# Kernel tuning notes

Hardware: AMD Instinct MI355X
Metric: run time of the kernel (lower is better)

The kernel has to match this reference:

```python
import jax, jax.numpy as jnp
import numpy as np

D_MODEL = 1024
NUM_HEADS = 16
D_K = D_MODEL // NUM_HEADS
NEG = -10000.0


def setup_inputs() -> dict:
    key = jax.random.key(0)
    ks = jax.random.split(key, 8)
    B, S = 2, 2048
    query = jax.random.normal(ks[0], (B, S, D_MODEL), dtype=jnp.float32)
    key_t = jax.random.normal(ks[1], (B, S, D_MODEL), dtype=jnp.float32)
    value = jax.random.normal(ks[2], (B, S, D_MODEL), dtype=jnp.float32)
    mask = jax.random.randint(ks[3], (B, S), 0, 2, dtype=jnp.int32)
    scale = 1.0 / np.sqrt(D_MODEL)
    Wq = jax.random.normal(ks[4], (D_MODEL, D_MODEL), dtype=jnp.float32) * scale
    Wk = jax.random.normal(ks[5], (D_MODEL, D_MODEL), dtype=jnp.float32) * scale
    Wv = jax.random.normal(ks[6], (D_MODEL, D_MODEL), dtype=jnp.float32) * scale
    Wo = jax.random.normal(ks[7], (D_MODEL, D_MODEL), dtype=jnp.float32) * scale
    return {"query": query, "key": key_t, "value": value, "mask": mask,
            "Wq": Wq, "Wk": Wk, "Wv": Wv, "Wo": Wo}


def reference(query, key, value, mask, Wq, Wk, Wv, Wo):
    B, Sq, _ = query.shape
    Sk = key.shape[1]
    # Linear projections (torch Linear: x @ W.T), split heads -> [B,H,S,d_k]
    def proj(x, W, S):
        return (x @ W.T).reshape(B, S, NUM_HEADS, D_K).transpose(0, 2, 1, 3)
    Q = proj(query, Wq, Sq)
    K = proj(key, Wk, Sk)
    V = proj(value, Wv, Sk)
    # scores [B,H,Sq,Sk]
    scores = jnp.einsum("bhqd,bhkd->bhqk", Q, K) / jnp.sqrt(jnp.float32(D_K))
    # padding mask [B,Sk] -> [B,1,1,Sk]
    pad = mask[:, None, None, :]
    scores = jnp.where(pad == 0, NEG, scores)
    # causal mask (mask_future=True)
    causal = jnp.tril(jnp.ones((Sq, Sk), dtype=bool))
    scores = jnp.where(causal, scores, NEG)
    probs = jax.nn.softmax(scores, axis=-1)  # dropout p=0.0 -> identity
    out = jnp.einsum("bhqk,bhkd->bhqd", probs, V)
    out = out.transpose(0, 2, 1, 3).reshape(B, Sq, D_MODEL)
    return out @ Wo.T
```

## Files before the change

kernel.cpp:

```cpp
#include <hip/hip_runtime.h>
#include <hip/hip_bf16.h>

typedef __attribute__((ext_vector_type(8))) short s16x8;
typedef __attribute__((ext_vector_type(4))) float f32x4;

#define MFMA16(a,b,c) __builtin_amdgcn_mfma_f32_16x16x32_bf16((a),(b),(c),0,0,0)

#define GLD16(gp, lp) __builtin_amdgcn_global_load_lds( \
  (const __attribute__((address_space(1))) unsigned int*)(gp), \
  (__attribute__((address_space(3))) unsigned int*)(lp), 16, 0, 0)

static __device__ __forceinline__ unsigned short f2bu(float f) {
  __hip_bfloat16 h = __float2bfloat16(f);
  unsigned short u; __builtin_memcpy(&u, &h, 2); return u;
}
static __device__ __forceinline__ float b2f(unsigned short u) {
  unsigned int x = ((unsigned int)u) << 16; float f; __builtin_memcpy(&f, &x, 4); return f;
}

__global__ __launch_bounds__(256) void cast_w4(const float* __restrict__ w0, const float* __restrict__ w1,
                                               const float* __restrict__ w2, const float* __restrict__ w3,
                                               unsigned short* __restrict__ o0, unsigned short* __restrict__ o1,
                                               unsigned short* __restrict__ o2, unsigned short* __restrict__ o3) {
  const int y = blockIdx.y;
  const float* in = (y == 0) ? w0 : (y == 1) ? w1 : (y == 2) ? w2 : w3;
  unsigned short* out = (y == 0) ? o0 : (y == 1) ? o1 : (y == 2) ? o2 : o3;
  int i = blockIdx.x * 256 + threadIdx.x;
  float4 v = *(const float4*)(in + (size_t)i * 4);
  unsigned int p0 = (unsigned int)f2bu(v.x) | ((unsigned int)f2bu(v.y) << 16);
  unsigned int p1 = (unsigned int)f2bu(v.z) | ((unsigned int)f2bu(v.w) << 16);
  uint2 pk; pk.x = p0; pk.y = p1;
  *(uint2*)(out + (size_t)i * 4) = pk;
}

static __device__ __forceinline__ void gemm_core(const float* __restrict__ A,
                                                 const unsigned short* __restrict__ Bw,
                                                 int m0, int n0,
                                                 f32x4 (&acc)[4][4],
                                                 unsigned short (*As)[64], unsigned short (*Bs)[64]) {
  const int K = 1024;
  const int tid = threadIdx.x;
  const int lane = tid & 63, wave = tid >> 6;
  const int wm = wave >> 1, wn = wave & 1;
  const int row16 = lane & 15, kgrp = lane >> 4;
  const int srow = lane >> 3, sslot = (lane & 7) ^ srow;
  const int sw = row16 & 7;

  for (int k0 = 0; k0 < K; k0 += 64) {
#pragma unroll
    for (int i = 0; i < 4; i++) {
      int rr = (wave * 4 + i) * 8 + srow;
      GLD16(Bw + (size_t)(n0 + rr) * K + k0 + sslot * 8,
            (char*)Bs + (wave * 4 + i) * 1024);
    }
    const float* Ag = A + (size_t)m0 * K + k0;
#pragma unroll
    for (int i = 0; i < 8; i++) {
      int f = tid + i * 256;
      int r = f >> 4, c = f & 15;
      float4 v = *(const float4*)(Ag + (size_t)r * K + c * 4);
      unsigned int p0 = (unsigned int)f2bu(v.x) | ((unsigned int)f2bu(v.y) << 16);
      unsigned int p1 = (unsigned int)f2bu(v.z) | ((unsigned int)f2bu(v.w) << 16);
      uint2 pk; pk.x = p0; pk.y = p1;
      int slot = (c >> 1) ^ (r & 7), half = c & 1;
      *(uint2*)((char*)&As[r][0] + slot * 16 + half * 8) = pk;
    }
    __syncthreads();

#pragma unroll
    for (int kk = 0; kk < 2; kk++) {
      s16x8 af[4], bfr[4];
#pragma unroll
      for (int mi = 0; mi < 4; mi++) {
        int rr = wm * 64 + mi * 16 + row16;
        af[mi] = *(const s16x8*)((char*)&As[rr][0] + ((kk * 4 + kgrp) ^ sw) * 16);
      }
#pragma unroll
      for (int ni = 0; ni < 4; ni++) {
        int rr = wn * 64 + ni * 16 + row16;
        bfr[ni] = *(const s16x8*)((char*)&Bs[rr][0] + ((kk * 4 + kgrp) ^ sw) * 16);
      }
#pragma unroll
      for (int mi = 0; mi < 4; mi++)
#pragma unroll
        for (int ni = 0; ni < 4; ni++)
          acc[mi][ni] = MFMA16(af[mi], bfr[ni], acc[mi][ni]);
    }
    __syncthreads();
  }
}

__global__ __launch_bounds__(256) void qkv_gemm(const float* __restrict__ q, const float* __restrict__ k,
                                                const float* __restrict__ v,
                                                const unsigned short* __restrict__ Wqb,
                                                const unsigned short* __restrict__ Wkb,
                                                const unsigned short* __restrict__ Wvb,
                                                unsigned short* __restrict__ Qb,
                                                unsigned short* __restrict__ Kb,
                                                unsigned short* __restrict__ Vt) {
  __shared__ unsigned short As[128][64];
  __shared__ unsigned short Bs[128][64];
  const int xcd = blockIdx.x & 7, u = blockIdx.x >> 3;
  const int g = xcd * 12 + (u >> 3);
  const int z = g >> 5, mstrip = g & 31;
  const int m0 = mstrip * 128, n0 = (u & 7) * 128;

  const float* A = (z == 0) ? q : (z == 1) ? k : v;
  const unsigned short* Bw = (z == 0) ? Wqb : (z == 1) ? Wkb : Wvb;

  f32x4 acc[4][4] = {};
  gemm_core(A, Bw, m0, n0, acc, As, Bs);

  const int lane = threadIdx.x & 63, wave = threadIdx.x >> 6;
  const int wm = wave >> 1, wn = wave & 1;
  const int row16 = lane & 15, kgrp = lane >> 4;

  if (z < 2) {
    unsigned short* C = z ? Kb : Qb;
#pragma unroll
    for (int mi = 0; mi < 4; mi++)
#pragma unroll
      for (int ni = 0; ni < 4; ni++)
#pragma unroll
        for (int r = 0; r < 4; r++) {
          int row = m0 + wm * 64 + mi * 16 + kgrp * 4 + r;
          int col = n0 + wn * 64 + ni * 16 + row16;
          C[(size_t)row * 1024 + col] = f2bu(acc[mi][ni][r]);
        }
  } else {
#pragma unroll
    for (int mi = 0; mi < 4; mi++)
#pragma unroll
      for (int ni = 0; ni < 4; ni++) {
        int mb = m0 + wm * 64 + mi * 16 + kgrp * 4;
        int col = n0 + wn * 64 + ni * 16 + row16;
        int bb = mb >> 11, s = mb & 2047;
        unsigned int p0 = (unsigned int)f2bu(acc[mi][ni][0]) | ((unsigned int)f2bu(acc[mi][ni][1]) << 16);
        unsigned int p1 = (unsigned int)f2bu(acc[mi][ni][2]) | ((unsigned int)f2bu(acc[mi][ni][3]) << 16);
        uint2 pk; pk.x = p0; pk.y = p1;
        *(uint2*)&Vt[(((size_t)(bb * 1024 + col)) << 11) + s] = pk;
      }
  }
}

__global__ __launch_bounds__(256) void gemm_wo(const float* __restrict__ A,
                                               const unsigned short* __restrict__ Bw,
                                               float* __restrict__ C) {
  __shared__ unsigned short As[128][64];
  __shared__ unsigned short Bs[128][64];
  const int xcd = blockIdx.x & 7, u = blockIdx.x >> 3;
  const int g = xcd * 4 + (u >> 3);
  const int m0 = g * 128, n0 = (u & 7) * 128;

  f32x4 acc[4][4] = {};
  gemm_core(A, Bw, m0, n0, acc, As, Bs);

  const int lane = threadIdx.x & 63, wave = threadIdx.x >> 6;
  const int wm = wave >> 1, wn = wave & 1;
  const int row16 = lane & 15, kgrp = lane >> 4;
#pragma unroll
  for (int mi = 0; mi < 4; mi++)
#pragma unroll
    for (int ni = 0; ni < 4; ni++)
#pragma unroll
      for (int r = 0; r < 4; r++) {
        int row = m0 + wm * 64 + mi * 16 + kgrp * 4 + r;
        int col = n0 + wn * 64 + ni * 16 + row16;
        C[(size_t)row * 1024 + col] = acc[mi][ni][r];
      }
}

__global__ __launch_bounds__(256) void fu_kernel(const int* __restrict__ mask, int* __restrict__ fu) {
  const int S = 2048;
  int b = blockIdx.x;
  __shared__ int red[256];
  int best = S;
  for (int k = threadIdx.x; k < S; k += 256)
    if (mask[b * S + k] != 0 && k < best) best = k;
  red[threadIdx.x] = best;
  __syncthreads();
  for (int s = 128; s > 0; s >>= 1) {
    if (threadIdx.x < s) red[threadIdx.x] = min(red[threadIdx.x], red[threadIdx.x + s]);
    __syncthreads();
  }
  if (threadIdx.x == 0) fu[b] = red[0];
}

__global__ __launch_bounds__(256) void reduce_vt(const unsigned short* __restrict__ Vt,
                                                 float* __restrict__ vsum) {
  __shared__ float red[256];
  const unsigned short* p = Vt + ((size_t)blockIdx.x << 11) + threadIdx.x * 8;
  uint4 u = *(const uint4*)p;
  float s = b2f((unsigned short)(u.x & 0xffff));
  s += b2f((unsigned short)(u.x >> 16));
  s += b2f((unsigned short)(u.y & 0xffff));
  s += b2f((unsigned short)(u.y >> 16));
  s += b2f((unsigned short)(u.z & 0xffff));
  s += b2f((unsigned short)(u.z >> 16));
  s += b2f((unsigned short)(u.w & 0xffff));
  s += b2f((unsigned short)(u.w >> 16));
  red[threadIdx.x] = s;
  __syncthreads();
  for (int st = 128; st > 0; st >>= 1) {
    if (threadIdx.x < st) red[threadIdx.x] += red[threadIdx.x + st];
    __syncthreads();
  }
  if (threadIdx.x == 0) vsum[blockIdx.x] = red[0];
}

__global__ __launch_bounds__(256) void flash_attn4(const unsigned short* __restrict__ Q,
                                                   const unsigned short* __restrict__ Kp,
                                                   const unsigned short* __restrict__ Vt,
                                                   const int* __restrict__ mask,
                                                   const int* __restrict__ fu,
                                                   const float* __restrict__ vsum,
                                                   float* __restrict__ O) {
  const int S = 2048, DM = 1024;
  const int xcd = blockIdx.x & 7, idx = blockIdx.x >> 3;
  const int bh = xcd * 4 + (idx >> 4);
  const int pairq = idx & 15;
  const int b = bh >> 4, h = bh & 15;
  const int tid = threadIdx.x, lane = tid & 63, wave = tid >> 6;
  const int row16 = lane & 15, kgrp = lane >> 4;

  __shared__ unsigned short Ks[2][64][64];
  __shared__ unsigned short Vs[2][64][64];
  __shared__ unsigned short Ps[4][16][72];

  const size_t base = ((size_t)b * S) * DM + h * 64;
  const size_t vtb = ((size_t)(b * 1024 + h * 64)) * S;
  const int* maskb = mask + b * S;

  const int srow = lane >> 3;
  const int sslot = (lane & 7) ^ srow;

  const int fub = fu[b];
  const float* vs = vsum + b * DM + h * 64;
  const int sw = row16 & 7;

#pragma unroll
  for (int pass = 0; pass < 2; ++pass) {
    const int qt = pass ? (31 - pairq) : pairq;
    const int q0 = qt * 64 + wave * 16;
    const int qg = q0 + row16;
    const int nt = qt + 1;

    s16x8 qf0 = *(const s16x8*)&Q[base + (size_t)qg * DM + kgrp * 8];
    s16x8 qf1 = *(const s16x8*)&Q[base + (size_t)qg * DM + 32 + kgrp * 8];

    f32x4 oacc[4] = {};
    float m_run = -1e30f, l_run = 0.f;

    auto stage = [&](int t, int bf) {
      const int kb = t * 64;
#pragma unroll
      for (int c2 = 0; c2 < 2; c2++) {
        const int r = wave * 16 + c2 * 8 + srow;
        GLD16(Kp + base + (size_t)(kb + r) * DM + sslot * 8,
              (char*)&Ks[bf][0][0] + (wave * 2 + c2) * 1024);
        GLD16(Vt + vtb + (size_t)r * S + kb + sslot * 8,
              (char*)&Vs[bf][0][0] + (wave * 2 + c2) * 1024);
      }
    };

    stage(0, 0);
    asm volatile("s_waitcnt vmcnt(0)" ::: "memory");
    __syncthreads();

    int cur = 0;
    for (int t = 0; t < nt; ++t) {
      if (t + 1 < nt) stage(t + 1, cur ^ 1);
      const int kb = t * 64;

      f32x4 sc[4];
#pragma unroll
      for (int nf = 0; nf < 4; nf++) {
        const int rr = nf * 16 + row16;
        s16x8 k0 = *(const s16x8*)&Ks[cur][rr][(kgrp ^ sw) * 8];
        s16x8 k1 = *(const s16x8*)&Ks[cur][rr][((4 + kgrp) ^ sw) * 8];
        f32x4 a = {};
        a = MFMA16(k0, qf0, a);
        a = MFMA16(k1, qf1, a);
        sc[nf] = a;
      }

#pragma unroll
      for (int nf = 0; nf < 4; nf++) {
        const int kbase = kb + nf * 16 + kgrp * 4;
        int4 mv = *(const int4*)&maskb[kbase];
#pragma unroll
        for (int r = 0; r < 4; r++) {
          int m_ok = (r == 0) ? mv.x : (r == 1) ? mv.y : (r == 2) ? mv.z : mv.w;
          float s = sc[nf][r] * 0.125f;
          sc[nf][r] = (kbase + r > qg || m_ok == 0) ? -10000.0f : s;
        }
      }

      float t01 = fmaxf(fmaxf(sc[0][0], sc[0][1]), fmaxf(sc[0][2], sc[0][3]));
      float t23 = fmaxf(fmaxf(sc[1][0], sc[1][1]), fmaxf(sc[1][2], sc[1][3]));
      float t45 = fmaxf(fmaxf(sc[2][0], sc[2][1]), fmaxf(sc[2][2], sc[2][3]));
      float t67 = fmaxf(fmaxf(sc[3][0], sc[3][1]), fmaxf(sc[3][2], sc[3][3]));
      float tmax = fmaxf(fmaxf(t01, t23), fmaxf(t45, t67));
      tmax = fmaxf(tmax, __shfl_xor(tmax, 16));
      tmax = fmaxf(tmax, __shfl_xor(tmax, 32));

      float mnew = fmaxf(m_run, tmax);
      float alpha = __expf(m_run - mnew);
      m_run = mnew;

      float rsum = 0.f;
#pragma unroll
      for (int nf = 0; nf < 4; nf++)
#pragma unroll
        for (int r = 0; r < 4; r++) {
          float p = __expf(sc[nf][r] - mnew);
          sc[nf][r] = p;
          rsum += p;
        }
      rsum += __shfl_xor(rsum, 16);
      rsum += __shfl_xor(rsum, 32);
      l_run = l_run * alpha + rsum;
#pragma unroll
      for (int nf2 = 0; nf2 < 4; nf2++)
#pragma unroll
        for (int r = 0; r < 4; r++) oacc[nf2][r] *= alpha;

#pragma unroll
      for (int nf = 0; nf < 4; nf++) {
        uint2 pk;
        pk.x = (unsigned int)f2bu(sc[nf][0]) | ((unsigned int)f2bu(sc[nf][1]) << 16);
        pk.y = (unsigned int)f2bu(sc[nf][2]) | ((unsigned int)f2bu(sc[nf][3]) << 16);
        *(uint2*)&Ps[wave][row16][nf * 16 + kgrp * 4] = pk;
      }
      s16x8 pf0 = *(const s16x8*)&Ps[wave][row16][kgrp * 8];
      s16x8 pf1 = *(const s16x8*)&Ps[wave][row16][32 + kgrp * 8];

#pragma unroll
      for (int nf2 = 0; nf2 < 4; nf2++) {
        const int rr = nf2 * 16 + row16;
        s16x8 v0 = *(const s16x8*)&Vs[cur][rr][(kgrp ^ sw) * 8];
        s16x8 v1 = *(const s16x8*)&Vs[cur][rr][((4 + kgrp) ^ sw) * 8];
        oacc[nf2] = MFMA16(v0, pf0, oacc[nf2]);
        oacc[nf2] = MFMA16(v1, pf1, oacc[nf2]);
      }

      asm volatile("s_waitcnt vmcnt(0)" ::: "memory");
      __syncthreads();
      cur ^= 1;
    }

    const float rl = 1.0f / l_run;
#pragma unroll
    for (int nf2 = 0; nf2 < 4; nf2++) {
      const int d0 = nf2 * 16 + kgrp * 4;
      float4 val;
      val.x = oacc[nf2][0] * rl;
      val.y = oacc[nf2][1] * rl;
      val.z = oacc[nf2][2] * rl;
      val.w = oacc[nf2][3] * rl;
      if (qg < fub) {
        float4 vv = *(const float4*)&vs[d0];
        val.x = vv.x * (1.0f / 2048.0f);
        val.y = vv.y * (1.0f / 2048.0f);
        val.z = vv.z * (1.0f / 2048.0f);
        val.w = vv.w * (1.0f / 2048.0f);
      }
      *(float4*)&O[base + (size_t)qg * DM + d0] = val;
    }
  }
}

extern "C" void kernel_launch(void* const* d_in, const int* in_sizes, int n_in,
                              void* d_out, int out_size, void* d_ws, size_t ws_size,
                              hipStream_t stream) {
  const float* q    = (const float*)d_in[0];
  const float* k    = (const float*)d_in[1];
  const float* v    = (const float*)d_in[2];
  const int*   mask = (const int*)d_in[3];
  const float* Wq   = (const float*)d_in[4];
  const float* Wk   = (const float*)d_in[5];
  const float* Wv   = (const float*)d_in[6];
  const float* Wo   = (const float*)d_in[7];
  float* out = (float*)d_out;
  char* ws = (char*)d_ws;

  unsigned short* Wqb = (unsigned short*)(ws + (size_t)0);
  unsigned short* Wkb = (unsigned short*)(ws + ((size_t)2 << 20));
  unsigned short* Wvb = (unsigned short*)(ws + ((size_t)4 << 20));
  unsigned short* Wob = (unsigned short*)(ws + ((size_t)6 << 20));
  unsigned short* Qb  = (unsigned short*)(ws + ((size_t)8 << 20));
  unsigned short* Kb  = (unsigned short*)(ws + ((size_t)16 << 20));
  unsigned short* Vt  = (unsigned short*)(ws + ((size_t)24 << 20));
  float* attn = (float*)(ws + ((size_t)32 << 20));
  float* vsum = (float*)(ws + ((size_t)48 << 20));
  int*   fub  = (int*)(ws + ((size_t)48 << 20) + (64 << 10));

  cast_w4<<<dim3(1024, 4), 256, 0, stream>>>(Wq, Wk, Wv, Wo, Wqb, Wkb, Wvb, Wob);

  qkv_gemm<<<768, 256, 0, stream>>>(q, k, v, Wqb, Wkb, Wvb, Qb, Kb, Vt);

  fu_kernel<<<2, 256, 0, stream>>>(mask, fub);
  reduce_vt<<<2048, 256, 0, stream>>>(Vt, vsum);

  flash_attn4<<<512, 256, 0, stream>>>(Qb, Kb, Vt, mask, fub, vsum, attn);

  gemm_wo<<<256, 256, 0, stream>>>(attn, Wob, out);
}
```

Before: 159.4 us.

## Pre-cast activations to bf16 and use async LDS loads for both GEMM operands

Adds a single cast kernel that converts q, k, v and all weights to bf16 up front, so gemm_core loads both A and B through global_load_lds instead of loading fp32 A, converting per tile and storing to LDS. The attention output is now written as bf16, which halves its write and the Wo GEMM read. The trade is an extra full read and write pass over the inputs, with buffers aliased into d_out and the workspace. Each A tile was previously reloaded and reconverted once per N tile, so the GEMMs should now be bandwidth-cheaper.

```diff
diff --git a/kernel.cpp b/kernel.cpp
--- a/kernel.cpp
+++ b/kernel.cpp
@@ -18,22 +18,36 @@
   unsigned int x = ((unsigned int)u) << 16; float f; __builtin_memcpy(&f, &x, 4); return f;
 }
 
-__global__ __launch_bounds__(256) void cast_w4(const float* __restrict__ w0, const float* __restrict__ w1,
-                                               const float* __restrict__ w2, const float* __restrict__ w3,
-                                               unsigned short* __restrict__ o0, unsigned short* __restrict__ o1,
-                                               unsigned short* __restrict__ o2, unsigned short* __restrict__ o3) {
+__global__ __launch_bounds__(256) void cast_all(const float* __restrict__ q, const float* __restrict__ k,
+                                                const float* __restrict__ v,
+                                                const float* __restrict__ Wq, const float* __restrict__ Wk,
+                                                const float* __restrict__ Wv, const float* __restrict__ Wo,
+                                                unsigned short* __restrict__ qc, unsigned short* __restrict__ kc,
+                                                unsigned short* __restrict__ vc,
+                                                unsigned short* __restrict__ wq, unsigned short* __restrict__ wk,
+                                                unsigned short* __restrict__ wv, unsigned short* __restrict__ wo) {
   const int y = blockIdx.y;
-  const float* in = (y == 0) ? w0 : (y == 1) ? w1 : (y == 2) ? w2 : w3;
-  unsigned short* out = (y == 0) ? o0 : (y == 1) ? o1 : (y == 2) ? o2 : o3;
+  const float* in; unsigned short* out; int n4;
+  switch (y) {
+    case 0: in = q;  out = qc; n4 = 1048576; break;
+    case 1: in = k;  out = kc; n4 = 1048576; break;
+    case 2: in = v;  out = vc; n4 = 1048576; break;
+    case 3: in = Wq; out = wq; n4 = 262144; break;
+    case 4: in = Wk; out = wk; n4 = 262144; break;
+    case 5: in = Wv; out = wv; n4 = 262144; break;
+    default: in = Wo; out = wo; n4 = 262144; break;
+  }
   int i = blockIdx.x * 256 + threadIdx.x;
-  float4 v = *(const float4*)(in + (size_t)i * 4);
-  unsigned int p0 = (unsigned int)f2bu(v.x) | ((unsigned int)f2bu(v.y) << 16);
-  unsigned int p1 = (unsigned int)f2bu(v.z) | ((unsigned int)f2bu(v.w) << 16);
-  uint2 pk; pk.x = p0; pk.y = p1;
-  *(uint2*)(out + (size_t)i * 4) = pk;
-}
-
-static __device__ __forceinline__ void gemm_core(const float* __restrict__ A,
+  if (i < n4) {
+    float4 val = *(const float4*)(in + (size_t)i * 4);
+    unsigned int p0 = (unsigned int)f2bu(val.x) | ((unsigned int)f2bu(val.y) << 16);
+    unsigned int p1 = (unsigned int)f2bu(val.z) | ((unsigned int)f2bu(val.w) << 16);
+    uint2 pk; pk.x = p0; pk.y = p1;
+    *(uint2*)(out + (size_t)i * 4) = pk;
+  }
+}
+
+static __device__ __forceinline__ void gemm_core(const unsigned short* __restrict__ Aw,
                                                  const unsigned short* __restrict__ Bw,
                                                  int m0, int n0,
                                                  f32x4 (&acc)[4][4],
@@ -50,20 +64,8 @@
 #pragma unroll
     for (int i = 0; i < 4; i++) {
       int rr = (wave * 4 + i) * 8 + srow;
-      GLD16(Bw + (size_t)(n0 + rr) * K + k0 + sslot * 8,
-            (char*)Bs + (wave * 4 + i) * 1024);
-    }
-    const float* Ag = A + (size_t)m0 * K + k0;
-#pragma unroll
-    for (int i = 0; i < 8; i++) {
-      int f = tid + i * 256;
-      int r = f >> 4, c = f & 15;
-      float4 v = *(const float4*)(Ag + (size_t)r * K + c * 4);
-      unsigned int p0 = (unsigned int)f2bu(v.x) | ((unsigned int)f2bu(v.y) << 16);
-      unsigned int p1 = (unsigned int)f2bu(v.z) | ((unsigned int)f2bu(v.w) << 16);
-      uint2 pk; pk.x = p0; pk.y = p1;
-      int slot = (c >> 1) ^ (r & 7), half = c & 1;
-      *(uint2*)((char*)&As[r][0] + slot * 16 + half * 8) = pk;
+      GLD16(Aw + (size_t)(m0 + rr) * K + k0 + sslot * 8, (char*)As + (wave * 4 + i) * 1024);
+      GLD16(Bw + (size_t)(n0 + rr) * K + k0 + sslot * 8, (char*)Bs + (wave * 4 + i) * 1024);
     }
     __syncthreads();
 
@@ -90,8 +92,9 @@
   }
 }
 
-__global__ __launch_bounds__(256) void qkv_gemm(const float* __restrict__ q, const float* __restrict__ k,
-                                                const float* __restrict__ v,
+__global__ __launch_bounds__(256) void qkv_gemm(const unsigned short* __restrict__ qc,
+                                                const unsigned short* __restrict__ kc,
+                                                const unsigned short* __restrict__ vc,
                                                 const unsigned short* __restrict__ Wqb,
                                                 const unsigned short* __restrict__ Wkb,
                                                 const unsigned short* __restrict__ Wvb,
@@ -105,7 +108,7 @@
   const int z = g >> 5, mstrip = g & 31;
   const int m0 = mstrip * 128, n0 = (u & 7) * 128;
 
-  const float* A = (z == 0) ? q : (z == 1) ? k : v;
+  const unsigned short* A = (z == 0) ? qc : (z == 1) ? kc : vc;
   const unsigned short* Bw = (z == 0) ? Wqb : (z == 1) ? Wkb : Wvb;
 
   f32x4 acc[4][4] = {};
@@ -143,7 +146,7 @@
   }
 }
 
-__global__ __launch_bounds__(256) void gemm_wo(const float* __restrict__ A,
+__global__ __launch_bounds__(256) void gemm_wo(const unsigned short* __restrict__ A,
                                                const unsigned short* __restrict__ Bw,
                                                float* __restrict__ C) {
   __shared__ unsigned short As[128][64];
@@ -214,7 +217,7 @@
                                                    const int* __restrict__ mask,
                                                    const int* __restrict__ fu,
                                                    const float* __restrict__ vsum,
-                                                   float* __restrict__ O) {
+                                                   unsigned short* __restrict__ O) {
   const int S = 2048, DM = 1024;
   const int xcd = blockIdx.x & 7, idx = blockIdx.x >> 3;
   const int bh = xcd * 4 + (idx >> 4);
@@ -353,19 +356,19 @@
 #pragma unroll
     for (int nf2 = 0; nf2 < 4; nf2++) {
       const int d0 = nf2 * 16 + kgrp * 4;
-      float4 val;
-      val.x = oacc[nf2][0] * rl;
-      val.y = oacc[nf2][1] * rl;
-      val.z = oacc[nf2][2] * rl;
-      val.w = oacc[nf2][3] * rl;
+      float v0 = oacc[nf2][0] * rl, v1 = oacc[nf2][1] * rl;
+      float v2 = oacc[nf2][2] * rl, v3 = oacc[nf2][3] * rl;
       if (qg < fub) {
         float4 vv = *(const float4*)&vs[d0];
-        val.x = vv.x * (1.0f / 2048.0f);
-        val.y = vv.y * (1.0f / 2048.0f);
-        val.z = vv.z * (1.0f / 2048.0f);
-        val.w = vv.w * (1.0f / 2048.0f);
-      }
-      *(float4*)&O[base + (size_t)qg * DM + d0] = val;
+        v0 = vv.x * (1.0f / 2048.0f);
+        v1 = vv.y * (1.0f / 2048.0f);
+        v2 = vv.z * (1.0f / 2048.0f);
+        v3 = vv.w * (1.0f / 2048.0f);
+      }
+      uint2 pk;
+      pk.x = (unsigned int)f2bu(v0) | ((unsigned int)f2bu(v1) << 16);
+      pk.y = (unsigned int)f2bu(v2) | ((unsigned int)f2bu(v3) << 16);
+      *(uint2*)&O[base + (size_t)qg * DM + d0] = pk;
     }
   }
 }
@@ -384,20 +387,24 @@
   float* out = (float*)d_out;
   char* ws = (char*)d_ws;
 
-  unsigned short* Wqb = (unsigned short*)(ws + (size_t)0);
-  unsigned short* Wkb = (unsigned short*)(ws + ((size_t)2 << 20));
-  unsigned short* Wvb = (unsigned short*)(ws + ((size_t)4 << 20));
-  unsigned short* Wob = (unsigned short*)(ws + ((size_t)6 << 20));
-  unsigned short* Qb  = (unsigned short*)(ws + ((size_t)8 << 20));
-  unsigned short* Kb  = (unsigned short*)(ws + ((size_t)16 << 20));
-  unsigned short* Vt  = (unsigned short*)(ws + ((size_t)24 << 20));
-  float* attn = (float*)(ws + ((size_t)32 << 20));
-  float* vsum = (float*)(ws + ((size_t)48 << 20));
-  int*   fub  = (int*)(ws + ((size_t)48 << 20) + (64 << 10));
-
-  cast_w4<<<dim3(1024, 4), 256, 0, stream>>>(Wq, Wk, Wv, Wo, Wqb, Wkb, Wvb, Wob);
-
-  qkv_gemm<<<768, 256, 0, stream>>>(q, k, v, Wqb, Wkb, Wvb, Qb, Kb, Vt);
+  unsigned short* Wqb  = (unsigned short*)(ws + (size_t)0);
+  unsigned short* Wkb  = (unsigned short*)(ws + ((size_t)2 << 20));
+  unsigned short* Wvb  = (unsigned short*)(ws + ((size_t)4 << 20));
+  unsigned short* Wob  = (unsigned short*)(ws + ((size_t)6 << 20));
+  unsigned short* vc   = (unsigned short*)(ws + ((size_t)8 << 20));
+  unsigned short* attn = (unsigned short*)(ws + ((size_t)8 << 20));
+  unsigned short* Qb   = (unsigned short*)(ws + ((size_t)16 << 20));
+  unsigned short* Kb   = (unsigned short*)(ws + ((size_t)24 << 20));
+  unsigned short* Vt   = (unsigned short*)(ws + ((size_t)32 << 20));
+  float* vsum          = (float*)(ws + ((size_t)40 << 20));
+  int*   fub           = (int*)(ws + ((size_t)40 << 20) + (64 << 10));
+  unsigned short* qc   = (unsigned short*)d_out;
+  unsigned short* kc   = (unsigned short*)d_out + 4194304;
+
+  cast_all<<<dim3(4096, 7), 256, 0, stream>>>(q, k, v, Wq, Wk, Wv, Wo,
+                                              qc, kc, vc, Wqb, Wkb, Wvb, Wob);
+
+  qkv_gemm<<<768, 256, 0, stream>>>(qc, kc, vc, Wqb, Wkb, Wvb, Qb, Kb, Vt);
 
   fu_kernel<<<2, 256, 0, stream>>>(mask, fub);
   reduce_vt<<<2048, 256, 0, stream>>>(Vt, vsum);
```

Result: faster. 151.2 us (-5.1%).
